# Kernel optimization log

Measured on AMD Instinct MI355X. Metric: run time of the kernel, lower is better.

The kernel has to match this reference:

```python
import jax, jax.numpy as jnp
import numpy as np

D = 1024  # input_dim


def setup_inputs() -> dict:
    key = jax.random.key(0)
    ks = jax.random.split(key, 7)
    s = 1.0 / np.sqrt(D)
    x = jax.random.normal(ks[0], (4, 2048, D), dtype=jnp.float32)
    Wq = jax.random.uniform(ks[1], (D, D), jnp.float32, -s, s)
    bq = jax.random.uniform(ks[2], (D,), jnp.float32, -s, s)
    Wk = jax.random.uniform(ks[3], (D, D), jnp.float32, -s, s)
    bk = jax.random.uniform(ks[4], (D,), jnp.float32, -s, s)
    Wv = jax.random.uniform(ks[5], (D, D), jnp.float32, -s, s)
    bv = jax.random.uniform(ks[6], (D,), jnp.float32, -s, s)
    return {"x": x, "Wq": Wq, "bq": bq, "Wk": Wk, "bk": bk, "Wv": Wv, "bv": bv}


def reference(x, Wq, bq, Wk, bk, Wv, bv):
    # nn.Linear: x @ W.T + b
    q = jnp.einsum('bsd,ed->bse', x, Wq) + bq
    k = jnp.einsum('bsd,ed->bse', x, Wk) + bk
    v = jnp.einsum('bsd,ed->bse', x, Wv) + bv
    scale = 1.0 / jnp.sqrt(jnp.asarray(x.shape[-1], x.dtype))
    scores = jnp.einsum('bqe,bke->bqk', q, k) * scale  # [B,S,S]
    weights = jax.nn.softmax(scores, axis=-1)
    return jnp.einsum('bqk,bke->bqe', weights, v)
```

## Files before the change

kernel.cpp:

```cpp
#include <hip/hip_runtime.h>
#include <hip/hip_bf16.h>
#include <stdint.h>


typedef float f32x4 __attribute__((ext_vector_type(4)));
typedef short s16x8 __attribute__((ext_vector_type(8)));

__device__ __forceinline__ uint16_t f2bf(float f) {
    uint32_t u = __float_as_uint(f);
    u += 0x7fffu + ((u >> 16) & 1u);
    return (uint16_t)(u >> 16);
}

#define GLOAD16(gp, lp)                                                  \
    __builtin_amdgcn_global_load_lds(                                    \
        (const __attribute__((address_space(1))) uint32_t*)(gp),         \
        (__attribute__((address_space(3))) uint32_t*)(lp), 16, 0, 0)

enum { MODE_EXP = 0, MODE_PV = 1 };


__global__ __launch_bounds__(256, 2) void proj_qkv(
    const uint16_t* __restrict__ xb, const uint16_t* __restrict__ wqb,
    const uint16_t* __restrict__ wkb, const uint16_t* __restrict__ wvb,
    const float* __restrict__ bq, const float* __restrict__ bk,
    const float* __restrict__ bv,
    uint16_t* __restrict__ qb, uint16_t* __restrict__ kb,
    uint16_t* __restrict__ vtb)
{
    __shared__ __attribute__((aligned(16))) uint16_t As[128 * 32];
    __shared__ __attribute__((aligned(16))) uint16_t Bs[128 * 32];

    const int id = blockIdx.x;
    const int proj = id >> 9;
    const int r = id & 511;

    const uint16_t* A;
    const uint16_t* Bm;
    const float* bias;
    uint16_t* C;
    long long row0, col0;
    int ldC;
    float cscale;
    if (proj < 2) {
        A = xb; Bm = proj ? wkb : wqb; bias = proj ? bk : bq;
        C = proj ? kb : qb; ldC = 1024;
        cscale = proj ? 1.0f : 0.03125f;
        row0 = (long long)(r & 63) * 128;
        col0 = (long long)(r >> 6) * 128;
    } else {
        A = wvb; Bm = xb; bias = bv; C = vtb; ldC = 8192; cscale = 1.0f;
        row0 = (long long)(r & 7) * 128;
        col0 = (long long)(r >> 3) * 128;
    }

    const int t = threadIdx.x;
    const int wave = t >> 6, lane = t & 63;
    const int wm = (wave >> 1) * 64, wn = (wave & 1) * 64;
    const int lr = lane & 15;

    const int c0 = wave * 64 + lane;
    const int c1 = c0 + 256;
    const int kc0 = ((c0 & 3) ^ ((c0 >> 3) & 3)) * 8;
    const int kc1 = ((c1 & 3) ^ ((c1 >> 3) & 3)) * 8;
    const uint16_t* gA0 = A  + (row0 + (c0 >> 2)) * 1024 + kc0;
    const uint16_t* gA1 = A  + (row0 + (c1 >> 2)) * 1024 + kc1;
    const uint16_t* gB0 = Bm + (col0 + (c0 >> 2)) * 1024 + kc0;
    const uint16_t* gB1 = Bm + (col0 + (c1 >> 2)) * 1024 + kc1;
    uint16_t* lA0 = As + wave * 512;
    uint16_t* lA1 = As + wave * 512 + 2048;
    uint16_t* lB0 = Bs + wave * 512;
    uint16_t* lB1 = Bs + wave * 512 + 2048;

    const int lka = (((lane >> 4) ^ ((lr >> 1) & 3))) * 8;

    f32x4 acc[4][4] = {};

    for (int k0 = 0; k0 < 1024; k0 += 32) {
        GLOAD16(gA0 + k0, lA0);
        GLOAD16(gA1 + k0, lA1);
        GLOAD16(gB0 + k0, lB0);
        GLOAD16(gB1 + k0, lB1);
        __syncthreads();

        s16x8 a[4], b[4];
#pragma unroll
        for (int i = 0; i < 4; ++i)
            a[i] = *(const s16x8*)(As + (wm + i * 16 + lr) * 32 + lka);
#pragma unroll
        for (int j = 0; j < 4; ++j)
            b[j] = *(const s16x8*)(Bs + (wn + j * 16 + lr) * 32 + lka);
#pragma unroll
        for (int i = 0; i < 4; ++i)
#pragma unroll
            for (int j = 0; j < 4; ++j)
                acc[i][j] = __builtin_amdgcn_mfma_f32_16x16x32_bf16(
                    a[i], b[j], acc[i][j], 0, 0, 0);
        __syncthreads();
    }

    const int rbase = wm + (lane >> 4) * 4;
    const int cbase = wn + lr;
    if (proj < 2) {
#pragma unroll
        for (int i = 0; i < 4; ++i)
#pragma unroll
            for (int rr = 0; rr < 4; ++rr) {
                const long long row = row0 + rbase + i * 16 + rr;
#pragma unroll
                for (int j = 0; j < 4; ++j) {
                    const long long col = col0 + cbase + j * 16;
                    C[row * ldC + col] = f2bf((acc[i][j][rr] + bias[col]) * cscale);
                }
            }
    } else {
#pragma unroll
        for (int i = 0; i < 4; ++i)
#pragma unroll
            for (int rr = 0; rr < 4; ++rr) {
                const long long row = row0 + rbase + i * 16 + rr;
                const float bb = bias[row];
#pragma unroll
                for (int j = 0; j < 4; ++j) {
                    const long long col = col0 + cbase + j * 16;
                    C[row * ldC + col] = f2bf(acc[i][j][rr] + bb);
                }
            }
    }
}

template <int MODE>
__global__ __launch_bounds__(256, 2) void gemm_bt(
    const uint16_t* __restrict__ A, int ldA, long long sA,
    const uint16_t* __restrict__ B, int ldB, long long sB,
    void* __restrict__ Cv, int ldC, long long sC,
    float* __restrict__ aux, int sAux, int K)
{
    __shared__ __attribute__((aligned(16))) uint16_t As[128 * 64];
    __shared__ __attribute__((aligned(16))) uint16_t Bs[128 * 64];

    const int z = blockIdx.z;
    const uint16_t* Ab = A + (long long)z * sA;
    const uint16_t* Bb = B + (long long)z * sB;
    float* ax = aux + (long long)z * sAux;

    const int t = threadIdx.x;
    const int wave = t >> 6, lane = t & 63;
    const int wm = (wave >> 1) * 64, wn = (wave & 1) * 64;
    const int lr = lane & 15;
    const long long row0 = (long long)blockIdx.x * 128;
    const long long col0 = (long long)blockIdx.y * 128;

    const uint16_t* gA[4]; const uint16_t* gB[4];
    uint16_t* lA[4]; uint16_t* lB[4];
#pragma unroll
    for (int p = 0; p < 4; ++p) {
        const int cs = p * 256 + wave * 64 + lane;
        const int rr = cs >> 3;
        const int kc = ((cs & 7) ^ (rr & 7)) * 8;
        gA[p] = Ab + (row0 + rr) * ldA + kc;
        gB[p] = Bb + (col0 + rr) * ldB + kc;
        lA[p] = As + (p * 256 + wave * 64) * 8;
        lB[p] = Bs + (p * 256 + wave * 64) * 8;
    }

    const int lr7 = lr & 7;

    f32x4 acc[4][4] = {};

    for (int k0 = 0; k0 < K; k0 += 64) {
#pragma unroll
        for (int p = 0; p < 4; ++p) GLOAD16(gA[p] + k0, lA[p]);
#pragma unroll
        for (int p = 0; p < 4; ++p) GLOAD16(gB[p] + k0, lB[p]);
        __syncthreads();

#pragma unroll
        for (int kk = 0; kk < 2; ++kk) {
            const int lka = ((kk * 4 + (lane >> 4)) ^ lr7) * 8;
            s16x8 a[4], b[4];
#pragma unroll
            for (int i = 0; i < 4; ++i)
                a[i] = *(const s16x8*)(As + (wm + i * 16 + lr) * 64 + lka);
#pragma unroll
            for (int j = 0; j < 4; ++j)
                b[j] = *(const s16x8*)(Bs + (wn + j * 16 + lr) * 64 + lka);
#pragma unroll
            for (int i = 0; i < 4; ++i)
#pragma unroll
                for (int j = 0; j < 4; ++j)
                    acc[i][j] = __builtin_amdgcn_mfma_f32_16x16x32_bf16(
                        a[i], b[j], acc[i][j], 0, 0, 0);
        }
        __syncthreads();
    }

    const int rbase = wm + (lane >> 4) * 4;
    const int cbase = wn + lr;

    if (MODE == MODE_EXP) {
        uint16_t* C = (uint16_t*)Cv + (long long)z * sC;
#pragma unroll
        for (int i = 0; i < 4; ++i)
#pragma unroll
            for (int rr = 0; rr < 4; ++rr) {
                const long long row = row0 + rbase + i * 16 + rr;
                float s = 0.f;
#pragma unroll
                for (int j = 0; j < 4; ++j) {
                    const long long col = col0 + cbase + j * 16;
                    const float val = __expf(acc[i][j][rr]);
                    C[row * ldC + col] = f2bf(val);
                    s += val;
                }
                s += __shfl_xor(s, 1);
                s += __shfl_xor(s, 2);
                s += __shfl_xor(s, 4);
                s += __shfl_xor(s, 8);
                if (lr == 0) atomicAdd(&ax[row], s);
            }
    } else {
        float* C = (float*)Cv + (long long)z * sC;
#pragma unroll
        for (int i = 0; i < 4; ++i)
#pragma unroll
            for (int rr = 0; rr < 4; ++rr) {
                const long long row = row0 + rbase + i * 16 + rr;
                const float linv = __builtin_amdgcn_rcpf(ax[row]);
#pragma unroll
                for (int j = 0; j < 4; ++j) {
                    const long long col = col0 + cbase + j * 16;
                    C[row * ldC + col] = acc[i][j][rr] * linv;
                }
            }
    }
}

__global__ void cast_all(const float* __restrict__ x, const float* __restrict__ Wq,
                         const float* __restrict__ Wk, const float* __restrict__ Wv,
                         uint16_t* __restrict__ xb, uint16_t* __restrict__ wqb,
                         uint16_t* __restrict__ wkb, uint16_t* __restrict__ wvb,
                         float* __restrict__ sums) {
    const int b = blockIdx.x;
    const float* in;
    uint16_t* out;
    int i;
    if (b < 8192)       { in = x;  out = xb;  i = b * 256 + threadIdx.x; }
    else if (b < 9216)  { in = Wq; out = wqb; i = (b - 8192) * 256 + threadIdx.x; }
    else if (b < 10240) { in = Wk; out = wkb; i = (b - 9216) * 256 + threadIdx.x; }
    else if (b < 11264) { in = Wv; out = wvb; i = (b - 10240) * 256 + threadIdx.x; }
    else {
        int j = (b - 11264) * 256 + threadIdx.x;
        ((float4*)sums)[j] = make_float4(0.f, 0.f, 0.f, 0.f);
        return;
    }
    float4 v = ((const float4*)in)[i];
    ushort4 o = make_ushort4(f2bf(v.x), f2bf(v.y), f2bf(v.z), f2bf(v.w));
    ((ushort4*)out)[i] = o;
}

extern "C" void kernel_launch(void* const* d_in, const int* in_sizes, int n_in,
                              void* d_out, int out_size, void* d_ws, size_t ws_size,
                              hipStream_t stream) {
    const float* x  = (const float*)d_in[0];
    const float* Wq = (const float*)d_in[1];
    const float* bq = (const float*)d_in[2];
    const float* Wk = (const float*)d_in[3];
    const float* bk = (const float*)d_in[4];
    const float* Wv = (const float*)d_in[5];
    const float* bv = (const float*)d_in[6];

    uint8_t* w = (uint8_t*)d_ws;
    uint16_t* xb  = (uint16_t*)w; w += (size_t)8192 * 1024 * 2;
    uint16_t* wqb = (uint16_t*)w; w += (size_t)1024 * 1024 * 2;
    uint16_t* wkb = (uint16_t*)w; w += (size_t)1024 * 1024 * 2;
    uint16_t* wvb = (uint16_t*)w; w += (size_t)1024 * 1024 * 2;
    uint16_t* qb  = (uint16_t*)w; w += (size_t)8192 * 1024 * 2;
    uint16_t* kb  = (uint16_t*)w; w += (size_t)8192 * 1024 * 2;
    uint16_t* vtb = (uint16_t*)w; w += (size_t)8192 * 1024 * 2;
    uint16_t* pb  = (uint16_t*)w; w += (size_t)4 * 2048 * 2048 * 2;
    float*    sums = (float*)w;  w += (size_t)8192 * 4;

    cast_all<<<dim3(11272), dim3(256), 0, stream>>>(x, Wq, Wk, Wv,
                                                    xb, wqb, wkb, wvb, sums);
    proj_qkv<<<dim3(1536), 256, 0, stream>>>(xb, wqb, wkb, wvb, bq, bk, bv,
                                             qb, kb, vtb);
    gemm_bt<MODE_EXP><<<dim3(16, 16, 4), 256, 0, stream>>>(
        qb, 1024, (long long)2048 * 1024, kb, 1024, (long long)2048 * 1024,
        pb, 2048, (long long)2048 * 2048, sums, 2048, 1024);
    gemm_bt<MODE_PV><<<dim3(16, 8, 4), 256, 0, stream>>>(
        pb, 2048, (long long)2048 * 2048, vtb, 8192, 2048,
        d_out, 1024, (long long)2048 * 1024, sums, 2048, 2048);
}
```

Measured before the change: 241.1 us.

## Share A tiles across two B tiles in QK projection and score GEMMs

The Q and K projections are fused into one block that loads each x tile once and multiplies it against both Wq and Wk tiles, with two accumulator sets. The score GEMM likewise computes a 128x256 output per block by reusing the Q tile against two K tiles. The projection k-step also grows from 32 to 64. This is meant to cut global and LDS traffic for the shared operand and halve the block count, at the cost of more registers and LDS per block, which may lower occupancy. V blocks now run with idle LDS and per-block imbalance.

```diff
diff --git a/kernel.cpp b/kernel.cpp
--- a/kernel.cpp
+++ b/kernel.cpp
@@ -16,8 +16,6 @@
     __builtin_amdgcn_global_load_lds(                                    \
         (const __attribute__((address_space(1))) uint32_t*)(gp),         \
         (__attribute__((address_space(3))) uint32_t*)(lp), 16, 0, 0)
-
-enum { MODE_EXP = 0, MODE_PV = 1 };
 
 
 __global__ __launch_bounds__(256, 2) void proj_qkv(
@@ -28,80 +26,95 @@
     uint16_t* __restrict__ qb, uint16_t* __restrict__ kb,
     uint16_t* __restrict__ vtb)
 {
-    __shared__ __attribute__((aligned(16))) uint16_t As[128 * 32];
-    __shared__ __attribute__((aligned(16))) uint16_t Bs[128 * 32];
+    __shared__ __attribute__((aligned(16))) uint16_t As[128 * 64];
+    __shared__ __attribute__((aligned(16))) uint16_t Bs1[128 * 64];
+    __shared__ __attribute__((aligned(16))) uint16_t Bs2[128 * 64];
 
     const int id = blockIdx.x;
-    const int proj = id >> 9;
-    const int r = id & 511;
-
-    const uint16_t* A;
-    const uint16_t* Bm;
-    const float* bias;
-    uint16_t* C;
-    long long row0, col0;
-    int ldC;
-    float cscale;
-    if (proj < 2) {
-        A = xb; Bm = proj ? wkb : wqb; bias = proj ? bk : bq;
-        C = proj ? kb : qb; ldC = 1024;
-        cscale = proj ? 1.0f : 0.03125f;
-        row0 = (long long)(r & 63) * 128;
-        col0 = (long long)(r >> 6) * 128;
-    } else {
-        A = wvb; Bm = xb; bias = bv; C = vtb; ldC = 8192; cscale = 1.0f;
-        row0 = (long long)(r & 7) * 128;
-        col0 = (long long)(r >> 3) * 128;
-    }
+    const bool qk = id < 512;
 
     const int t = threadIdx.x;
     const int wave = t >> 6, lane = t & 63;
     const int wm = (wave >> 1) * 64, wn = (wave & 1) * 64;
     const int lr = lane & 15;
-
-    const int c0 = wave * 64 + lane;
-    const int c1 = c0 + 256;
-    const int kc0 = ((c0 & 3) ^ ((c0 >> 3) & 3)) * 8;
-    const int kc1 = ((c1 & 3) ^ ((c1 >> 3) & 3)) * 8;
-    const uint16_t* gA0 = A  + (row0 + (c0 >> 2)) * 1024 + kc0;
-    const uint16_t* gA1 = A  + (row0 + (c1 >> 2)) * 1024 + kc1;
-    const uint16_t* gB0 = Bm + (col0 + (c0 >> 2)) * 1024 + kc0;
-    const uint16_t* gB1 = Bm + (col0 + (c1 >> 2)) * 1024 + kc1;
-    uint16_t* lA0 = As + wave * 512;
-    uint16_t* lA1 = As + wave * 512 + 2048;
-    uint16_t* lB0 = Bs + wave * 512;
-    uint16_t* lB1 = Bs + wave * 512 + 2048;
-
-    const int lka = (((lane >> 4) ^ ((lr >> 1) & 3))) * 8;
-
-    f32x4 acc[4][4] = {};
-
-    for (int k0 = 0; k0 < 1024; k0 += 32) {
-        GLOAD16(gA0 + k0, lA0);
-        GLOAD16(gA1 + k0, lA1);
-        GLOAD16(gB0 + k0, lB0);
-        GLOAD16(gB1 + k0, lB1);
-        __syncthreads();
-
-        s16x8 a[4], b[4];
-#pragma unroll
-        for (int i = 0; i < 4; ++i)
-            a[i] = *(const s16x8*)(As + (wm + i * 16 + lr) * 32 + lka);
-#pragma unroll
-        for (int j = 0; j < 4; ++j)
-            b[j] = *(const s16x8*)(Bs + (wn + j * 16 + lr) * 32 + lka);
-#pragma unroll
-        for (int i = 0; i < 4; ++i)
+    const int lr7 = lr & 7;
+
+    long long row0, col0;
+    const uint16_t *A, *B1, *B2;
+    if (qk) {
+        row0 = (long long)(id >> 3) * 128;
+        col0 = (long long)(id & 7) * 128;
+        A = xb; B1 = wqb; B2 = wkb;
+    } else {
+        const int vid = id - 512;
+        row0 = (long long)(vid & 7) * 128;
+        col0 = (long long)(vid >> 3) * 128;
+        A = wvb; B1 = xb; B2 = nullptr;
+    }
+
+    const uint16_t* gA[4]; const uint16_t* gB1[4]; const uint16_t* gB2[4];
+    uint16_t* lA[4]; uint16_t* lB1[4]; uint16_t* lB2[4];
+#pragma unroll
+    for (int p = 0; p < 4; ++p) {
+        const int cs = p * 256 + wave * 64 + lane;
+        const int rr = cs >> 3;
+        const int kc = ((cs & 7) ^ (rr & 7)) * 8;
+        gA[p]  = A  + (row0 + rr) * 1024 + kc;
+        gB1[p] = B1 + (col0 + rr) * 1024 + kc;
+        if (qk) gB2[p] = B2 + (col0 + rr) * 1024 + kc;
+        lA[p]  = As  + (p * 256 + wave * 64) * 8;
+        lB1[p] = Bs1 + (p * 256 + wave * 64) * 8;
+        lB2[p] = Bs2 + (p * 256 + wave * 64) * 8;
+    }
+
+    f32x4 acc1[4][4] = {};
+    f32x4 acc2[4][4] = {};
+
+    for (int k0 = 0; k0 < 1024; k0 += 64) {
+#pragma unroll
+        for (int p = 0; p < 4; ++p) GLOAD16(gA[p] + k0, lA[p]);
+#pragma unroll
+        for (int p = 0; p < 4; ++p) GLOAD16(gB1[p] + k0, lB1[p]);
+        if (qk) {
+#pragma unroll
+            for (int p = 0; p < 4; ++p) GLOAD16(gB2[p] + k0, lB2[p]);
+        }
+        __syncthreads();
+
+#pragma unroll
+        for (int kk = 0; kk < 2; ++kk) {
+            const int lka = ((kk * 4 + (lane >> 4)) ^ lr7) * 8;
+            s16x8 a[4], b[4];
+#pragma unroll
+            for (int i = 0; i < 4; ++i)
+                a[i] = *(const s16x8*)(As + (wm + i * 16 + lr) * 64 + lka);
 #pragma unroll
             for (int j = 0; j < 4; ++j)
-                acc[i][j] = __builtin_amdgcn_mfma_f32_16x16x32_bf16(
-                    a[i], b[j], acc[i][j], 0, 0, 0);
+                b[j] = *(const s16x8*)(Bs1 + (wn + j * 16 + lr) * 64 + lka);
+#pragma unroll
+            for (int i = 0; i < 4; ++i)
+#pragma unroll
+                for (int j = 0; j < 4; ++j)
+                    acc1[i][j] = __builtin_amdgcn_mfma_f32_16x16x32_bf16(
+                        a[i], b[j], acc1[i][j], 0, 0, 0);
+            if (qk) {
+#pragma unroll
+                for (int j = 0; j < 4; ++j)
+                    b[j] = *(const s16x8*)(Bs2 + (wn + j * 16 + lr) * 64 + lka);
+#pragma unroll
+                for (int i = 0; i < 4; ++i)
+#pragma unroll
+                    for (int j = 0; j < 4; ++j)
+                        acc2[i][j] = __builtin_amdgcn_mfma_f32_16x16x32_bf16(
+                            a[i], b[j], acc2[i][j], 0, 0, 0);
+            }
+        }
         __syncthreads();
     }
 
     const int rbase = wm + (lane >> 4) * 4;
     const int cbase = wn + lr;
-    if (proj < 2) {
+    if (qk) {
 #pragma unroll
         for (int i = 0; i < 4; ++i)
 #pragma unroll
@@ -110,7 +123,8 @@
 #pragma unroll
                 for (int j = 0; j < 4; ++j) {
                     const long long col = col0 + cbase + j * 16;
-                    C[row * ldC + col] = f2bf((acc[i][j][rr] + bias[col]) * cscale);
+                    qb[row * 1024 + col] = f2bf((acc1[i][j][rr] + bq[col]) * 0.03125f);
+                    kb[row * 1024 + col] = f2bf(acc2[i][j][rr] + bk[col]);
                 }
             }
     } else {
@@ -119,60 +133,64 @@
 #pragma unroll
             for (int rr = 0; rr < 4; ++rr) {
                 const long long row = row0 + rbase + i * 16 + rr;
-                const float bb = bias[row];
+                const float bb = bv[row];
 #pragma unroll
                 for (int j = 0; j < 4; ++j) {
                     const long long col = col0 + cbase + j * 16;
-                    C[row * ldC + col] = f2bf(acc[i][j][rr] + bb);
+                    vtb[row * 8192 + col] = f2bf(acc1[i][j][rr] + bb);
                 }
             }
     }
 }
 
-template <int MODE>
-__global__ __launch_bounds__(256, 2) void gemm_bt(
-    const uint16_t* __restrict__ A, int ldA, long long sA,
-    const uint16_t* __restrict__ B, int ldB, long long sB,
-    void* __restrict__ Cv, int ldC, long long sC,
-    float* __restrict__ aux, int sAux, int K)
+__global__ __launch_bounds__(256, 2) void gemm_exp(
+    const uint16_t* __restrict__ Q, const uint16_t* __restrict__ Km,
+    uint16_t* __restrict__ P, float* __restrict__ sums)
 {
     __shared__ __attribute__((aligned(16))) uint16_t As[128 * 64];
-    __shared__ __attribute__((aligned(16))) uint16_t Bs[128 * 64];
+    __shared__ __attribute__((aligned(16))) uint16_t Bs1[128 * 64];
+    __shared__ __attribute__((aligned(16))) uint16_t Bs2[128 * 64];
 
     const int z = blockIdx.z;
-    const uint16_t* Ab = A + (long long)z * sA;
-    const uint16_t* Bb = B + (long long)z * sB;
-    float* ax = aux + (long long)z * sAux;
+    const uint16_t* Ab = Q  + (long long)z * 2048 * 1024;
+    const uint16_t* Bb = Km + (long long)z * 2048 * 1024;
+    uint16_t* Cb = P + (long long)z * 2048 * 2048;
+    float* ax = sums + (long long)z * 2048;
 
     const int t = threadIdx.x;
     const int wave = t >> 6, lane = t & 63;
     const int wm = (wave >> 1) * 64, wn = (wave & 1) * 64;
     const int lr = lane & 15;
-    const long long row0 = (long long)blockIdx.x * 128;
-    const long long col0 = (long long)blockIdx.y * 128;
-
-    const uint16_t* gA[4]; const uint16_t* gB[4];
-    uint16_t* lA[4]; uint16_t* lB[4];
+    const int lr7 = lr & 7;
+    const long long row0  = (long long)blockIdx.x * 128;
+    const long long col0a = (long long)blockIdx.y * 256;
+    const long long col0b = col0a + 128;
+
+    const uint16_t* gA[4]; const uint16_t* gB1[4]; const uint16_t* gB2[4];
+    uint16_t* lA[4]; uint16_t* lB1[4]; uint16_t* lB2[4];
 #pragma unroll
     for (int p = 0; p < 4; ++p) {
         const int cs = p * 256 + wave * 64 + lane;
         const int rr = cs >> 3;
         const int kc = ((cs & 7) ^ (rr & 7)) * 8;
-        gA[p] = Ab + (row0 + rr) * ldA + kc;
-        gB[p] = Bb + (col0 + rr) * ldB + kc;
-        lA[p] = As + (p * 256 + wave * 64) * 8;
-        lB[p] = Bs + (p * 256 + wave * 64) * 8;
-    }
-
-    const int lr7 = lr & 7;
-
-    f32x4 acc[4][4] = {};
-
-    for (int k0 = 0; k0 < K; k0 += 64) {
+        gA[p]  = Ab + (row0  + rr) * 1024 + kc;
+        gB1[p] = Bb + (col0a + rr) * 1024 + kc;
+        gB2[p] = Bb + (col0b + rr) * 1024 + kc;
+        lA[p]  = As  + (p * 256 + wave * 64) * 8;
+        lB1[p] = Bs1 + (p * 256 + wave * 64) * 8;
+        lB2[p] = Bs2 + (p * 256 + wave * 64) * 8;
+    }
+
+    f32x4 acc1[4][4] = {};
+    f32x4 acc2[4][4] = {};
+
+    for (int k0 = 0; k0 < 1024; k0 += 64) {
 #pragma unroll
         for (int p = 0; p < 4; ++p) GLOAD16(gA[p] + k0, lA[p]);
 #pragma unroll
-        for (int p = 0; p < 4; ++p) GLOAD16(gB[p] + k0, lB[p]);
+        for (int p = 0; p < 4; ++p) GLOAD16(gB1[p] + k0, lB1[p]);
+#pragma unroll
+        for (int p = 0; p < 4; ++p) GLOAD16(gB2[p] + k0, lB2[p]);
         __syncthreads();
 
 #pragma unroll
@@ -184,6 +202,104 @@
                 a[i] = *(const s16x8*)(As + (wm + i * 16 + lr) * 64 + lka);
 #pragma unroll
             for (int j = 0; j < 4; ++j)
+                b[j] = *(const s16x8*)(Bs1 + (wn + j * 16 + lr) * 64 + lka);
+#pragma unroll
+            for (int i = 0; i < 4; ++i)
+#pragma unroll
+                for (int j = 0; j < 4; ++j)
+                    acc1[i][j] = __builtin_amdgcn_mfma_f32_16x16x32_bf16(
+                        a[i], b[j], acc1[i][j], 0, 0, 0);
+#pragma unroll
+            for (int j = 0; j < 4; ++j)
+                b[j] = *(const s16x8*)(Bs2 + (wn + j * 16 + lr) * 64 + lka);
+#pragma unroll
+            for (int i = 0; i < 4; ++i)
+#pragma unroll
+                for (int j = 0; j < 4; ++j)
+                    acc2[i][j] = __builtin_amdgcn_mfma_f32_16x16x32_bf16(
+                        a[i], b[j], acc2[i][j], 0, 0, 0);
+        }
+        __syncthreads();
+    }
+
+    const int rbase = wm + (lane >> 4) * 4;
+    const int cbase = wn + lr;
+#pragma unroll
+    for (int i = 0; i < 4; ++i)
+#pragma unroll
+        for (int rr = 0; rr < 4; ++rr) {
+            const long long row = row0 + rbase + i * 16 + rr;
+            float s = 0.f;
+#pragma unroll
+            for (int j = 0; j < 4; ++j) {
+                const long long ca = col0a + cbase + j * 16;
+                const long long cb2 = col0b + cbase + j * 16;
+                const float va = __expf(acc1[i][j][rr]);
+                const float vb = __expf(acc2[i][j][rr]);
+                Cb[row * 2048 + ca]  = f2bf(va);
+                Cb[row * 2048 + cb2] = f2bf(vb);
+                s += va + vb;
+            }
+            s += __shfl_xor(s, 1);
+            s += __shfl_xor(s, 2);
+            s += __shfl_xor(s, 4);
+            s += __shfl_xor(s, 8);
+            if (lr == 0) atomicAdd(&ax[row], s);
+        }
+}
+
+__global__ __launch_bounds__(256, 2) void gemm_pv(
+    const uint16_t* __restrict__ P, const uint16_t* __restrict__ Vt,
+    float* __restrict__ Out, const float* __restrict__ sums)
+{
+    __shared__ __attribute__((aligned(16))) uint16_t As[128 * 64];
+    __shared__ __attribute__((aligned(16))) uint16_t Bs[128 * 64];
+
+    const int z = blockIdx.z;
+    const uint16_t* Ab = P + (long long)z * 2048 * 2048;
+    const uint16_t* Bb = Vt + (long long)z * 2048;
+    float* Cb = Out + (long long)z * 2048 * 1024;
+    const float* ax = sums + (long long)z * 2048;
+
+    const int t = threadIdx.x;
+    const int wave = t >> 6, lane = t & 63;
+    const int wm = (wave >> 1) * 64, wn = (wave & 1) * 64;
+    const int lr = lane & 15;
+    const int lr7 = lr & 7;
+    const long long row0 = (long long)blockIdx.x * 128;
+    const long long col0 = (long long)blockIdx.y * 128;
+
+    const uint16_t* gA[4]; const uint16_t* gB[4];
+    uint16_t* lA[4]; uint16_t* lB[4];
+#pragma unroll
+    for (int p = 0; p < 4; ++p) {
+        const int cs = p * 256 + wave * 64 + lane;
+        const int rr = cs >> 3;
+        const int kc = ((cs & 7) ^ (rr & 7)) * 8;
+        gA[p] = Ab + (row0 + rr) * 2048 + kc;
+        gB[p] = Bb + (col0 + rr) * 8192 + kc;
+        lA[p] = As + (p * 256 + wave * 64) * 8;
+        lB[p] = Bs + (p * 256 + wave * 64) * 8;
+    }
+
+    f32x4 acc[4][4] = {};
+
+    for (int k0 = 0; k0 < 2048; k0 += 64) {
+#pragma unroll
+        for (int p = 0; p < 4; ++p) GLOAD16(gA[p] + k0, lA[p]);
+#pragma unroll
+        for (int p = 0; p < 4; ++p) GLOAD16(gB[p] + k0, lB[p]);
+        __syncthreads();
+
+#pragma unroll
+        for (int kk = 0; kk < 2; ++kk) {
+            const int lka = ((kk * 4 + (lane >> 4)) ^ lr7) * 8;
+            s16x8 a[4], b[4];
+#pragma unroll
+            for (int i = 0; i < 4; ++i)
+                a[i] = *(const s16x8*)(As + (wm + i * 16 + lr) * 64 + lka);
+#pragma unroll
+            for (int j = 0; j < 4; ++j)
                 b[j] = *(const s16x8*)(Bs + (wn + j * 16 + lr) * 64 + lka);
 #pragma unroll
             for (int i = 0; i < 4; ++i)
@@ -197,43 +313,18 @@
 
     const int rbase = wm + (lane >> 4) * 4;
     const int cbase = wn + lr;
-
-    if (MODE == MODE_EXP) {
-        uint16_t* C = (uint16_t*)Cv + (long long)z * sC;
-#pragma unroll
-        for (int i = 0; i < 4; ++i)
-#pragma unroll
-            for (int rr = 0; rr < 4; ++rr) {
-                const long long row = row0 + rbase + i * 16 + rr;
-                float s = 0.f;
-#pragma unroll
-                for (int j = 0; j < 4; ++j) {
-                    const long long col = col0 + cbase + j * 16;
-                    const float val = __expf(acc[i][j][rr]);
-                    C[row * ldC + col] = f2bf(val);
-                    s += val;
-                }
-                s += __shfl_xor(s, 1);
-                s += __shfl_xor(s, 2);
-                s += __shfl_xor(s, 4);
-                s += __shfl_xor(s, 8);
-                if (lr == 0) atomicAdd(&ax[row], s);
-            }
-    } else {
-        float* C = (float*)Cv + (long long)z * sC;
-#pragma unroll
-        for (int i = 0; i < 4; ++i)
-#pragma unroll
-            for (int rr = 0; rr < 4; ++rr) {
-                const long long row = row0 + rbase + i * 16 + rr;
-                const float linv = __builtin_amdgcn_rcpf(ax[row]);
-#pragma unroll
-                for (int j = 0; j < 4; ++j) {
-                    const long long col = col0 + cbase + j * 16;
-                    C[row * ldC + col] = acc[i][j][rr] * linv;
-                }
-            }
-    }
+#pragma unroll
+    for (int i = 0; i < 4; ++i)
+#pragma unroll
+        for (int rr = 0; rr < 4; ++rr) {
+            const long long row = row0 + rbase + i * 16 + rr;
+            const float linv = __builtin_amdgcn_rcpf(ax[row]);
+#pragma unroll
+            for (int j = 0; j < 4; ++j) {
+                const long long col = col0 + cbase + j * 16;
+                Cb[row * 1024 + col] = acc[i][j][rr] * linv;
+            }
+        }
 }
 
 __global__ void cast_all(const float* __restrict__ x, const float* __restrict__ Wq,
@@ -283,12 +374,8 @@
 
     cast_all<<<dim3(11272), dim3(256), 0, stream>>>(x, Wq, Wk, Wv,
                                                     xb, wqb, wkb, wvb, sums);
-    proj_qkv<<<dim3(1536), 256, 0, stream>>>(xb, wqb, wkb, wvb, bq, bk, bv,
+    proj_qkv<<<dim3(1024), 256, 0, stream>>>(xb, wqb, wkb, wvb, bq, bk, bv,
                                              qb, kb, vtb);
-    gemm_bt<MODE_EXP><<<dim3(16, 16, 4), 256, 0, stream>>>(
-        qb, 1024, (long long)2048 * 1024, kb, 1024, (long long)2048 * 1024,
-        pb, 2048, (long long)2048 * 2048, sums, 2048, 1024);
-    gemm_bt<MODE_PV><<<dim3(16, 8, 4), 256, 0, stream>>>(
-        pb, 2048, (long long)2048 * 2048, vtb, 8192, 2048,
-        d_out, 1024, (long long)2048 * 1024, sums, 2048, 2048);
-}
+    gemm_exp<<<dim3(16, 8, 4), 256, 0, stream>>>(qb, kb, pb, sums);
+    gemm_pv<<<dim3(16, 8, 4), 256, 0, stream>>>(pb, vtb, (float*)d_out, sums);
+}
```

New measurement: 234.6 us. 1.03x faster.
